# Kernel optimization log

Measured on AMD Instinct MI355X. Metric: run time of the kernel, lower is better.

The kernel has to match this reference:

```python
import jax, jax.numpy as jnp
import numpy as np

N_USER = 50000
N_ITEM = 100000
N = N_USER + N_ITEM
D = 64
NNZ = 2_400_000
B = 4096
N_LAYERS = 3
NEG_SLOPE = 0.01  # F.leaky_relu default
EPS = 1e-12       # F.normalize default eps


def setup_inputs() -> dict:
    key = jax.random.key(0)
    ks = jax.random.split(key, 12)
    s = 0.1  # xavier-ish scale
    return {
        "user_emb": jax.random.normal(ks[0], (N_USER, D), jnp.float32) * s,
        "item_emb": jax.random.normal(ks[1], (N_ITEM, D), jnp.float32) * s,
        "W_gc": jax.random.normal(ks[2], (N_LAYERS, D, D), jnp.float32) * s,
        "W_bi": jax.random.normal(ks[3], (N_LAYERS, D, D), jnp.float32) * s,
        "b_bi": jax.random.normal(ks[4], (N_LAYERS, 1, D), jnp.float32) * s,
        "vals": jax.random.uniform(ks[5], (NNZ,), jnp.float32) * (1.0 / 16.0),
        "rows": jax.random.randint(ks[6], (NNZ,), 0, N, jnp.int32),
        "cols": jax.random.randint(ks[7], (NNZ,), 0, N, jnp.int32),
        "users": jax.random.randint(ks[8], (B,), 0, N_USER, jnp.int32),
        "pos_items": jax.random.randint(ks[9], (B,), 0, N_ITEM, jnp.int32),
        "neg_items": jax.random.randint(ks[10], (B,), 0, N_ITEM, jnp.int32),
    }


def _spmm(rows, cols, vals, E, n):
    # sparse [n,n] (COO) @ dense [n,d]
    return jax.ops.segment_sum(vals[:, None] * E[cols], rows, num_segments=n)


def reference(user_emb, item_emb, W_gc, W_bi, b_bi, vals, rows, cols,
              users, pos_items, neg_items):
    n_user = user_emb.shape[0]
    n = n_user + item_emb.shape[0]
    ego = jnp.concatenate([user_emb, item_emb], axis=0)  # [N, D]
    all_embs = [ego]
    for k in range(N_LAYERS):
        L_side = _spmm(rows, cols, vals, ego, n)        # L @ E
        LI_side = L_side + ego                           # (L + I) @ E
        # NOTE: original code adds b_bi to BOTH branches (b_gc unused)
        sum_e = LI_side @ W_gc[k] + b_bi[k]
        bi_e = (L_side * ego) @ W_bi[k] + b_bi[k]
        ego = jax.nn.leaky_relu(sum_e + bi_e, NEG_SLOPE)
        norm = ego / jnp.maximum(
            jnp.linalg.norm(ego, axis=1, keepdims=True), EPS)
        all_embs.append(norm)
    all_embs = jnp.concatenate(all_embs, axis=1)         # [N, D*(L+1)]
    u_g = all_embs[:n_user][users]
    pos_g = all_embs[n_user:][pos_items]
    neg_g = all_embs[n_user:][neg_items]
    return (u_g, pos_g, neg_g)
```

## Files before the change

kernel.cpp:

```cpp
#include <hip/hip_runtime.h>

#define N_USER 50000
#define N_ITEM 100000
#define NTOT   150000
#define D      64
#define NNZ    2400000
#define NEG_SLOPE 0.01f

#define BSHIFT 10
#define NB     147
#define P1_PER 4096
#define NBLK1  586
#define NROWBLK 2344

typedef unsigned int uint;
typedef unsigned short ushort;
typedef _Float16 h2 __attribute__((ext_vector_type(2)));
typedef _Float16 h4 __attribute__((ext_vector_type(4)));
typedef float f4 __attribute__((ext_vector_type(4)));

__global__ void k_concat16(const float* __restrict__ u, const float* __restrict__ it,
                           ushort* __restrict__ A16, int* __restrict__ bcnt) {
    if (blockIdx.x == 0 && threadIdx.x < NB) bcnt[threadIdx.x] = 0;
    int i = blockIdx.x * 256 + threadIdx.x;
    const int nu4 = N_USER * D / 4;
    float4 v = (i < nu4) ? ((const float4*)u)[i] : ((const float4*)it)[i - nu4];
    h2 a, b;
    a.x = (_Float16)v.x; a.y = (_Float16)v.y;
    b.x = (_Float16)v.z; b.y = (_Float16)v.w;
    ((uint2*)A16)[i] = make_uint2(__builtin_bit_cast(uint, a), __builtin_bit_cast(uint, b));
}

__global__ __launch_bounds__(1024) void k_bhist(const int* __restrict__ rows,
                                                int* __restrict__ bcnt) {
    __shared__ int lcnt[NB];
    int tid = threadIdx.x;
    if (tid < NB) lcnt[tid] = 0;
    __syncthreads();
    int base = blockIdx.x * P1_PER;
    #pragma unroll
    for (int k = 0; k < 4; ++k) {
        int i = base + k * 1024 + tid;
        if (i < NNZ) atomicAdd(&lcnt[rows[i] >> BSHIFT], 1);
    }
    __syncthreads();
    if (tid < NB) atomicAdd(&bcnt[tid], lcnt[tid]);
}

__global__ void k_bscan_gather(const int* __restrict__ bcnt, int* __restrict__ bptr,
                               int* __restrict__ bcur,
                               const float* __restrict__ u, const float* __restrict__ it,
                               const int* __restrict__ users, const int* __restrict__ pos,
                               const int* __restrict__ neg, float* __restrict__ out) {
    __shared__ int s[256];
    if (blockIdx.x == 3072) {
        int tid = threadIdx.x;
        int v = (tid < NB) ? bcnt[tid] : 0;
        s[tid] = v; __syncthreads();
        for (int off = 1; off < 256; off <<= 1) {
            int t = (tid >= off) ? s[tid - off] : 0;
            __syncthreads();
            s[tid] += t;
            __syncthreads();
        }
        if (tid < NB) { int ex = s[tid] - v; bptr[tid] = ex; bcur[tid] = ex; }
        if (tid == NB - 1) bptr[NB] = s[tid];
        return;
    }
    int lane = threadIdx.x & 63;
    int gi = blockIdx.x * 4 + (threadIdx.x >> 6);
    int g = gi >> 12, b = gi & 4095;
    const float* src = (g == 0) ? (u + (size_t)users[b] * D)
                                : (it + (size_t)((g == 1) ? pos[b] : neg[b]) * D);
    out[gi * 256 + lane] = src[lane];
}

__global__ __launch_bounds__(1024) void k_binpass1(const int* __restrict__ rows,
                                                   const int* __restrict__ cols,
                                                   const float* __restrict__ vals,
                                                   int* __restrict__ bcur,
                                                   int2* __restrict__ bucketed) {
    __shared__ int lcnt[NB], lbase[NB];
    int tid = threadIdx.x;
    int base = blockIdx.x * P1_PER;
    if (tid < NB) lcnt[tid] = 0;
    __syncthreads();
    int r[4];
    #pragma unroll
    for (int k = 0; k < 4; ++k) {
        int i = base + k * 1024 + tid;
        r[k] = (i < NNZ) ? rows[i] : -1;
        if (r[k] >= 0) atomicAdd(&lcnt[r[k] >> BSHIFT], 1);
    }
    __syncthreads();
    if (tid < NB) { lbase[tid] = atomicAdd(&bcur[tid], lcnt[tid]); lcnt[tid] = 0; }
    __syncthreads();
    #pragma unroll
    for (int k = 0; k < 4; ++k) {
        int i = base + k * 1024 + tid;
        if (r[k] >= 0) {
            int b = r[k] >> BSHIFT;
            int off = atomicAdd(&lcnt[b], 1);
            bucketed[lbase[b] + off] =
                make_int2(((r[k] & 1023) << 18) | cols[i], __float_as_int(vals[i]));
        }
    }
}

__global__ __launch_bounds__(1024) void k_binpass2(const int* __restrict__ bptr,
                                                   const int2* __restrict__ bucketed,
                                                   int* __restrict__ ptr,
                                                   int2* __restrict__ csr) {
    __shared__ int c0[1024], px[1024];
    int tid = threadIdx.x, b = blockIdx.x;
    int s = bptr[b], e = bptr[b + 1];
    c0[tid] = 0;
    __syncthreads();
    for (int i = s + tid; i < e; i += 1024) atomicAdd(&c0[bucketed[i].x >> 18], 1);
    __syncthreads();
    int v = c0[tid];
    px[tid] = v;
    __syncthreads();
    for (int off = 1; off < 1024; off <<= 1) {
        int t = (tid >= off) ? px[tid - off] : 0;
        __syncthreads();
        px[tid] += t;
        __syncthreads();
    }
    int ex = px[tid] - v;
    int r = (b << BSHIFT) + tid;
    if (r <= NTOT) ptr[r] = s + ex;
    px[tid] = ex;
    c0[tid] = 0;
    __syncthreads();
    for (int i = s + tid; i < e; i += 1024) {
        int2 e2 = bucketed[i];
        int lr = e2.x >> 18;
        int off = atomicAdd(&c0[lr], 1);
        csr[s + px[lr] + off] = make_int2(e2.x & 0x3FFFF, e2.y);
    }
}

__global__ __launch_bounds__(256) void k_spmm(const int* __restrict__ ptr,
                                              const int2* __restrict__ csr,
                                              const ushort* __restrict__ E16,
                                              ushort* __restrict__ L16) {
    int lane = threadIdx.x & 63;
    int half = lane >> 5;
    int l32  = lane & 31;
    int r = __builtin_amdgcn_readfirstlane(blockIdx.x * 4 + (threadIdx.x >> 6));
    int start = ptr[r], end = ptr[r + 1];
    float acc0 = 0.f, acc1 = 0.f;
    const uint* E32 = (const uint*)E16;
    int j = start;
    for (; j + 15 < end; j += 16) {
        int2 ea0 = csr[j + 0],  ea1 = csr[j + 1],  ea2 = csr[j + 2],  ea3 = csr[j + 3];
        int2 ea4 = csr[j + 4],  ea5 = csr[j + 5],  ea6 = csr[j + 6],  ea7 = csr[j + 7];
        int2 ea8 = csr[j + 8],  ea9 = csr[j + 9],  eaA = csr[j + 10], eaB = csr[j + 11];
        int2 eaC = csr[j + 12], eaD = csr[j + 13], eaE = csr[j + 14], eaF = csr[j + 15];
        int c0 = half ? ea1.x : ea0.x;
        int c1 = half ? ea3.x : ea2.x;
        int c2 = half ? ea5.x : ea4.x;
        int c3 = half ? ea7.x : ea6.x;
        int c4 = half ? ea9.x : ea8.x;
        int c5 = half ? eaB.x : eaA.x;
        int c6 = half ? eaD.x : eaC.x;
        int c7 = half ? eaF.x : eaE.x;
        uint u0 = E32[(c0 << 5) + l32];
        uint u1 = E32[(c1 << 5) + l32];
        uint u2 = E32[(c2 << 5) + l32];
        uint u3 = E32[(c3 << 5) + l32];
        uint u4 = E32[(c4 << 5) + l32];
        uint u5 = E32[(c5 << 5) + l32];
        uint u6 = E32[(c6 << 5) + l32];
        uint u7 = E32[(c7 << 5) + l32];
        float v0 = __int_as_float(half ? ea1.y : ea0.y);
        float v1 = __int_as_float(half ? ea3.y : ea2.y);
        float v2 = __int_as_float(half ? ea5.y : ea4.y);
        float v3 = __int_as_float(half ? ea7.y : ea6.y);
        float v4 = __int_as_float(half ? ea9.y : ea8.y);
        float v5 = __int_as_float(half ? eaB.y : eaA.y);
        float v6 = __int_as_float(half ? eaD.y : eaC.y);
        float v7 = __int_as_float(half ? eaF.y : eaE.y);
        h2 p0 = __builtin_bit_cast(h2, u0), p1 = __builtin_bit_cast(h2, u1);
        h2 p2 = __builtin_bit_cast(h2, u2), p3 = __builtin_bit_cast(h2, u3);
        h2 p4 = __builtin_bit_cast(h2, u4), p5 = __builtin_bit_cast(h2, u5);
        h2 p6 = __builtin_bit_cast(h2, u6), p7 = __builtin_bit_cast(h2, u7);
        acc0 += v0 * (float)p0.x;  acc1 += v0 * (float)p0.y;
        acc0 += v1 * (float)p1.x;  acc1 += v1 * (float)p1.y;
        acc0 += v2 * (float)p2.x;  acc1 += v2 * (float)p2.y;
        acc0 += v3 * (float)p3.x;  acc1 += v3 * (float)p3.y;
        acc0 += v4 * (float)p4.x;  acc1 += v4 * (float)p4.y;
        acc0 += v5 * (float)p5.x;  acc1 += v5 * (float)p5.y;
        acc0 += v6 * (float)p6.x;  acc1 += v6 * (float)p6.y;
        acc0 += v7 * (float)p7.x;  acc1 += v7 * (float)p7.y;
    }
    for (; j + 7 < end; j += 8) {
        int2 ea = csr[j + 0], eb = csr[j + 1];
        int2 ec = csr[j + 2], ed = csr[j + 3];
        int2 ee = csr[j + 4], ef = csr[j + 5];
        int2 eg = csr[j + 6], eh = csr[j + 7];
        int c0 = half ? eb.x : ea.x;
        int c1 = half ? ed.x : ec.x;
        int c2 = half ? ef.x : ee.x;
        int c3 = half ? eh.x : eg.x;
        uint u0 = E32[(c0 << 5) + l32];
        uint u1 = E32[(c1 << 5) + l32];
        uint u2 = E32[(c2 << 5) + l32];
        uint u3 = E32[(c3 << 5) + l32];
        float v0 = __int_as_float(half ? eb.y : ea.y);
        float v1 = __int_as_float(half ? ed.y : ec.y);
        float v2 = __int_as_float(half ? ef.y : ee.y);
        float v3 = __int_as_float(half ? eh.y : eg.y);
        h2 p0 = __builtin_bit_cast(h2, u0), p1 = __builtin_bit_cast(h2, u1);
        h2 p2 = __builtin_bit_cast(h2, u2), p3 = __builtin_bit_cast(h2, u3);
        acc0 += v0 * (float)p0.x;  acc1 += v0 * (float)p0.y;
        acc0 += v1 * (float)p1.x;  acc1 += v1 * (float)p1.y;
        acc0 += v2 * (float)p2.x;  acc1 += v2 * (float)p2.y;
        acc0 += v3 * (float)p3.x;  acc1 += v3 * (float)p3.y;
    }
    for (; j + 1 < end; j += 2) {
        int2 ea = csr[j], eb = csr[j + 1];
        int c   = half ? eb.x : ea.x;
        float v = __int_as_float(half ? eb.y : ea.y);
        h2 p = __builtin_bit_cast(h2, E32[(c << 5) + l32]);
        acc0 += v * (float)p.x;  acc1 += v * (float)p.y;
    }
    if (j < end) {
        int2 ea = csr[j];
        if (half == 0) {
            h2 p = __builtin_bit_cast(h2, E32[(ea.x << 5) + l32]);
            float v = __int_as_float(ea.y);
            acc0 += v * (float)p.x;  acc1 += v * (float)p.y;
        }
    }
    acc0 += __shfl_xor(acc0, 32, 64);
    acc1 += __shfl_xor(acc1, 32, 64);
    if (half == 0) {
        h2 o; o.x = (_Float16)acc0; o.y = (_Float16)acc1;
        ((uint*)L16)[(r << 5) + l32] = __builtin_bit_cast(uint, o);
    }
}

__global__ __launch_bounds__(256) void k_transform_mfma(
        const ushort* __restrict__ E16, const ushort* __restrict__ L16,
        const float* __restrict__ Wgc, const float* __restrict__ Wbi,
        const float* __restrict__ bb, ushort* __restrict__ O16, int n) {
    __shared__ _Float16 ldsW[2 * 16 * 256];
    __shared__ ushort   ldsO[4][16 * 72];
    int tid = threadIdx.x;

    #pragma unroll
    for (int m = 0; m < 2; ++m) {
        const float* W = m ? Wbi : Wgc;
        for (int idx = tid; idx < 4096; idx += 256) {
            int k = idx >> 6, nn = idx & 63;
            ldsW[(m * 16 + (k >> 4) * 4 + (nn >> 4)) * 256 + (nn & 15) * 16 + (k & 15)] =
                (_Float16)W[idx];
        }
    }
    __syncthreads();

    int l = tid & 63, w = tid >> 6;
    int g = l >> 4, r16 = l & 15;

    h4 bfrag[2][4][4];
    #pragma unroll
    for (int m = 0; m < 2; ++m)
        #pragma unroll
        for (int ks = 0; ks < 4; ++ks)
            #pragma unroll
            for (int nt = 0; nt < 4; ++nt)
                bfrag[m][ks][nt] =
                    *(const h4*)&ldsW[(m * 16 + ks * 4 + nt) * 256 + r16 * 16 + g * 4];

    int rowbase = blockIdx.x * 64 + w * 16;
    int r = rowbase + r16;
    int rc = min(r, n - 1);

    h4 x1[4], x2[4];
    #pragma unroll
    for (int ks = 0; ks < 4; ++ks) {
        int ui = (rc << 5) + ks * 8 + g * 2;
        uint2 lw = *(const uint2*)&((const uint*)L16)[ui];
        uint2 ew = *(const uint2*)&((const uint*)E16)[ui];
        h4 l4, e4;
        h2 la = __builtin_bit_cast(h2, lw.x), lb = __builtin_bit_cast(h2, lw.y);
        h2 ea = __builtin_bit_cast(h2, ew.x), eb = __builtin_bit_cast(h2, ew.y);
        l4[0] = la.x; l4[1] = la.y; l4[2] = lb.x; l4[3] = lb.y;
        e4[0] = ea.x; e4[1] = ea.y; e4[2] = eb.x; e4[3] = eb.y;
        x1[ks] = l4 + e4;
        x2[ks] = l4 * e4;
    }

    f4 acc[4];
    #pragma unroll
    for (int nt = 0; nt < 4; ++nt) acc[nt] = (f4){0.f, 0.f, 0.f, 0.f};
    #pragma unroll
    for (int ks = 0; ks < 4; ++ks)
        #pragma unroll
        for (int nt = 0; nt < 4; ++nt)
            acc[nt] = __builtin_amdgcn_mfma_f32_16x16x16f16(x1[ks], bfrag[0][ks][nt],
                                                            acc[nt], 0, 0, 0);
    #pragma unroll
    for (int ks = 0; ks < 4; ++ks)
        #pragma unroll
        for (int nt = 0; nt < 4; ++nt)
            acc[nt] = __builtin_amdgcn_mfma_f32_16x16x16f16(x2[ks], bfrag[1][ks][nt],
                                                            acc[nt], 0, 0, 0);

    #pragma unroll
    for (int nt = 0; nt < 4; ++nt) {
        int col = nt * 16 + r16;
        float bv = 2.f * bb[col];
        #pragma unroll
        for (int i = 0; i < 4; ++i) {
            float y = acc[nt][i] + bv;
            y = (y >= 0.f) ? y : NEG_SLOPE * y;
            ldsO[w][(g * 4 + i) * 72 + col] = __builtin_bit_cast(ushort, (_Float16)y);
        }
    }
    int lr = l >> 2;
    int rowg = rowbase + lr;
    if (rowg < n) {
        const ushort* src = &ldsO[w][lr * 72 + (l & 3) * 16];
        uint4 v0 = *(const uint4*)src;
        uint4 v1 = *(const uint4*)(src + 8);
        *(uint4*)&O16[rowg * D + (l & 3) * 16] = v0;
        *(uint4*)&O16[rowg * D + (l & 3) * 16 + 8] = v1;
    }
}

__global__ void k_gathern(const ushort* __restrict__ E16, const int* __restrict__ users,
                          const int* __restrict__ pos, const int* __restrict__ neg,
                          float* __restrict__ out, int layer) {
    int lane = threadIdx.x & 63;
    int gi = blockIdx.x * 4 + (threadIdx.x >> 6);
    int g = gi >> 12, b = gi & 4095;
    int src = (g == 0) ? users[b] : (N_USER + ((g == 1) ? pos[b] : neg[b]));
    float v = (float)__builtin_bit_cast(_Float16, E16[src * D + lane]);
    float ss = v * v;
    #pragma unroll
    for (int off = 32; off >= 1; off >>= 1) ss += __shfl_xor(ss, off, 64);
    float dnm = fmaxf(sqrtf(ss), 1e-12f);
    out[gi * 256 + layer * D + lane] = v / dnm;
}

extern "C" void kernel_launch(void* const* d_in, const int* in_sizes, int n_in,
                              void* d_out, int out_size, void* d_ws, size_t ws_size,
                              hipStream_t stream) {
    const float* user_emb = (const float*)d_in[0];
    const float* item_emb = (const float*)d_in[1];
    const float* W_gc     = (const float*)d_in[2];
    const float* W_bi     = (const float*)d_in[3];
    const float* b_bi     = (const float*)d_in[4];
    const float* vals     = (const float*)d_in[5];
    const int*   rows     = (const int*)d_in[6];
    const int*   cols     = (const int*)d_in[7];
    const int*   users    = (const int*)d_in[8];
    const int*   pos      = (const int*)d_in[9];
    const int*   neg      = (const int*)d_in[10];
    float* out = (float*)d_out;

    char* ws = (char*)d_ws;
    size_t off = 0;
    auto alloc = [&](size_t b) { void* p = ws + off; off += (b + 255) & ~(size_t)255; return p; };
    ushort* Ea  = (ushort*)alloc((size_t)NTOT * D * 2);
    ushort* Eb  = (ushort*)alloc((size_t)NTOT * D * 2);
    ushort* L16 = (ushort*)alloc((size_t)NTOT * D * 2);
    int2*   csr = (int2*)  alloc((size_t)NNZ * 8);
    int*    ptr = (int*)   alloc((size_t)(NTOT + 64) * 4);
    int*    bptr= (int*)   alloc((NB + 1) * 4);
    int*    bcnt= (int*)   alloc(NB * 4);
    int*    bcur= (int*)   alloc(NB * 4);
    int2*   bucketed = (int2*)alloc((size_t)NNZ * 8);
    (void)ws_size;

    hipLaunchKernelGGL(k_concat16,    dim3(9375), dim3(256),  0, stream, user_emb, item_emb, Ea, bcnt);
    hipLaunchKernelGGL(k_bhist,       dim3(NBLK1),dim3(1024), 0, stream, rows, bcnt);
    hipLaunchKernelGGL(k_bscan_gather,dim3(3073), dim3(256),  0, stream, bcnt, bptr, bcur,
                       user_emb, item_emb, users, pos, neg, out);
    hipLaunchKernelGGL(k_binpass1,    dim3(NBLK1),dim3(1024), 0, stream, rows, cols, vals, bcur, bucketed);
    hipLaunchKernelGGL(k_binpass2,    dim3(NB),   dim3(1024), 0, stream, bptr, bucketed, ptr, csr);

    ushort* cur = Ea; ushort* nxt = Eb;
    for (int k = 0; k < 3; ++k) {
        hipLaunchKernelGGL(k_spmm,           dim3(37500),  dim3(256), 0, stream, ptr, csr, cur, L16);
        hipLaunchKernelGGL(k_transform_mfma, dim3(NROWBLK),dim3(256), 0, stream, cur, L16,
                           W_gc + k * 4096, W_bi + k * 4096, b_bi + k * 64, nxt, NTOT);
        hipLaunchKernelGGL(k_gathern,        dim3(3072),   dim3(256), 0, stream, nxt, users, pos, neg, out, k + 1);
        ushort* t = cur; cur = nxt; nxt = t;
    }
}
```

Measured before the change: 450.3 us.

## Fuse per-layer normalized gather into next SpMM launch and stage transform inputs in LDS

Removes the separate gather-normalize kernel after each layer. The gather for layer k is done by extra blocks appended to the layer k+1 SpMM grid, and only the final layer keeps a standalone gather launch. The transform kernel now loads L and E rows with coalesced 16-byte loads into a padded LDS staging buffer, reads the MFMA fragments from there, and reuses the same buffer for output staging after a barrier. This cuts two launches and improves global load coalescing, at the cost of more LDS traffic and an extra __syncthreads.

```diff
diff --git a/kernel.cpp b/kernel.cpp
--- a/kernel.cpp
+++ b/kernel.cpp
@@ -12,6 +12,7 @@
 #define P1_PER 4096
 #define NBLK1  586
 #define NROWBLK 2344
+#define SPMM_BLKS 37500
 
 typedef unsigned int uint;
 typedef unsigned short ushort;
@@ -144,8 +145,24 @@
 __global__ __launch_bounds__(256) void k_spmm(const int* __restrict__ ptr,
                                               const int2* __restrict__ csr,
                                               const ushort* __restrict__ E16,
-                                              ushort* __restrict__ L16) {
+                                              ushort* __restrict__ L16,
+                                              const int* __restrict__ users,
+                                              const int* __restrict__ pos,
+                                              const int* __restrict__ neg,
+                                              float* __restrict__ out, int layer) {
     int lane = threadIdx.x & 63;
+    if (blockIdx.x >= SPMM_BLKS) {
+        int gi = (blockIdx.x - SPMM_BLKS) * 4 + (threadIdx.x >> 6);
+        int g = gi >> 12, b = gi & 4095;
+        int src = (g == 0) ? users[b] : (N_USER + ((g == 1) ? pos[b] : neg[b]));
+        float v = (float)__builtin_bit_cast(_Float16, E16[src * D + lane]);
+        float ss = v * v;
+        #pragma unroll
+        for (int off = 32; off >= 1; off >>= 1) ss += __shfl_xor(ss, off, 64);
+        float dnm = fmaxf(sqrtf(ss), 1e-12f);
+        out[gi * 256 + layer * D + lane] = v / dnm;
+        return;
+    }
     int half = lane >> 5;
     int l32  = lane & 31;
     int r = __builtin_amdgcn_readfirstlane(blockIdx.x * 4 + (threadIdx.x >> 6));
@@ -242,12 +259,13 @@
     }
 }
 
+#define SPITCH 36
 __global__ __launch_bounds__(256) void k_transform_mfma(
         const ushort* __restrict__ E16, const ushort* __restrict__ L16,
         const float* __restrict__ Wgc, const float* __restrict__ Wbi,
         const float* __restrict__ bb, ushort* __restrict__ O16, int n) {
     __shared__ _Float16 ldsW[2 * 16 * 256];
-    __shared__ ushort   ldsO[4][16 * 72];
+    __shared__ __align__(16) uint stage[4][2 * 16 * SPITCH];
     int tid = threadIdx.x;
 
     #pragma unroll
@@ -275,15 +293,30 @@
                     *(const h4*)&ldsW[(m * 16 + ks * 4 + nt) * 256 + r16 * 16 + g * 4];
 
     int rowbase = blockIdx.x * 64 + w * 16;
-    int r = rowbase + r16;
-    int rc = min(r, n - 1);
+
+    uint* sL = &stage[w][0];
+    uint* sE = &stage[w][16 * SPITCH];
+    {
+        int sr = l >> 2;
+        int ch = (l & 3) * 8;
+        int rg = min(rowbase + sr, n - 1);
+        int gb = (rg << 5) + ch;
+        uint4 la = *(const uint4*)&((const uint*)L16)[gb];
+        uint4 lb = *(const uint4*)&((const uint*)L16)[gb + 4];
+        uint4 ea = *(const uint4*)&((const uint*)E16)[gb];
+        uint4 eb = *(const uint4*)&((const uint*)E16)[gb + 4];
+        *(uint4*)&sL[sr * SPITCH + ch]     = la;
+        *(uint4*)&sL[sr * SPITCH + ch + 4] = lb;
+        *(uint4*)&sE[sr * SPITCH + ch]     = ea;
+        *(uint4*)&sE[sr * SPITCH + ch + 4] = eb;
+    }
 
     h4 x1[4], x2[4];
     #pragma unroll
     for (int ks = 0; ks < 4; ++ks) {
-        int ui = (rc << 5) + ks * 8 + g * 2;
-        uint2 lw = *(const uint2*)&((const uint*)L16)[ui];
-        uint2 ew = *(const uint2*)&((const uint*)E16)[ui];
+        int si = r16 * SPITCH + ks * 8 + g * 2;
+        uint2 lw = *(const uint2*)&sL[si];
+        uint2 ew = *(const uint2*)&sE[si];
         h4 l4, e4;
         h2 la = __builtin_bit_cast(h2, lw.x), lb = __builtin_bit_cast(h2, lw.y);
         h2 ea = __builtin_bit_cast(h2, ew.x), eb = __builtin_bit_cast(h2, ew.y);
@@ -309,6 +342,9 @@
             acc[nt] = __builtin_amdgcn_mfma_f32_16x16x16f16(x2[ks], bfrag[1][ks][nt],
                                                             acc[nt], 0, 0, 0);
 
+    __syncthreads();
+
+    ushort* ow = (ushort*)&stage[w][0];
     #pragma unroll
     for (int nt = 0; nt < 4; ++nt) {
         int col = nt * 16 + r16;
@@ -317,13 +353,13 @@
         for (int i = 0; i < 4; ++i) {
             float y = acc[nt][i] + bv;
             y = (y >= 0.f) ? y : NEG_SLOPE * y;
-            ldsO[w][(g * 4 + i) * 72 + col] = __builtin_bit_cast(ushort, (_Float16)y);
+            ow[(g * 4 + i) * 72 + col] = __builtin_bit_cast(ushort, (_Float16)y);
         }
     }
     int lr = l >> 2;
     int rowg = rowbase + lr;
     if (rowg < n) {
-        const ushort* src = &ldsO[w][lr * 72 + (l & 3) * 16];
+        const ushort* src = &ow[lr * 72 + (l & 3) * 16];
         uint4 v0 = *(const uint4*)src;
         uint4 v1 = *(const uint4*)(src + 8);
         *(uint4*)&O16[rowg * D + (l & 3) * 16] = v0;
@@ -385,10 +421,12 @@
 
     ushort* cur = Ea; ushort* nxt = Eb;
     for (int k = 0; k < 3; ++k) {
-        hipLaunchKernelGGL(k_spmm,           dim3(37500),  dim3(256), 0, stream, ptr, csr, cur, L16);
-        hipLaunchKernelGGL(k_transform_mfma, dim3(NROWBLK),dim3(256), 0, stream, cur, L16,
+        int grid = (k == 0) ? SPMM_BLKS : SPMM_BLKS + 3072;
+        hipLaunchKernelGGL(k_spmm, dim3(grid), dim3(256), 0, stream, ptr, csr, cur, L16,
+                           users, pos, neg, out, k);
+        hipLaunchKernelGGL(k_transform_mfma, dim3(NROWBLK), dim3(256), 0, stream, cur, L16,
                            W_gc + k * 4096, W_bi + k * 4096, b_bi + k * 64, nxt, NTOT);
-        hipLaunchKernelGGL(k_gathern,        dim3(3072),   dim3(256), 0, stream, nxt, users, pos, neg, out, k + 1);
         ushort* t = cur; cur = nxt; nxt = t;
     }
-}
+    hipLaunchKernelGGL(k_gathern, dim3(3072), dim3(256), 0, stream, cur, users, pos, neg, out, 3);
+}
```

Result: no change. 444.9 us (-1.2%).
